# Kernel tuning notes

Measured on AMD Instinct MI355X. Metric: run time of the kernel, lower is better.

The kernel has to match this reference:

```python
import jax, jax.numpy as jnp
import numpy as np

B, C_I, C_O, K, H, W = 8, 64, 64, 3, 256, 256
GROUPS = 16  # int(c_o / min(4, c_o)) = 64/4
EPS = 1e-5
PAD = K  # pad_x = pad_y = k + (bc-1) with bc_x=bc_y=1, k=3


def _conv(x, w):
    # x: (B, C_i, h, w), w: (C_o, C_i, K, K), valid conv, stride 1
    return jax.lax.conv_general_dilated(
        x, w, window_strides=(1, 1), padding='VALID',
        dimension_numbers=('NCHW', 'OIHW', 'NCHW'))


def setup_inputs() -> dict:
    key = jax.random.key(0)
    ks = jax.random.split(key, 10)
    s = 1.0 / np.sqrt(C_I * K * K)  # torch Conv2d default init bound
    wshape = (C_O, C_I, K, K)
    names = ['w_int', 'w_tl', 'w_tr', 'w_bl', 'w_br', 'w_top', 'w_bot', 'w_left', 'w_right']
    d = {'x': jax.random.normal(ks[0], (B, C_I, H, W), dtype=jnp.float32)}
    for i, n in enumerate(names):
        d[n] = jax.random.uniform(ks[i + 1], wshape, jnp.float32, -s, s)
    d['bias'] = jnp.zeros((1, C_O, 1, 1), jnp.float32)   # learnable_bias (init zeros)
    d['gamma'] = jnp.ones((C_O,), jnp.float32)           # GroupNorm weight
    d['beta'] = jnp.zeros((C_O,), jnp.float32)           # GroupNorm bias
    return d


def reference(x, w_int, w_tl, w_tr, w_bl, w_br, w_top, w_bot, w_left, w_right, bias, gamma, beta):
    p = PAD
    # corners -> (B,C,1,1)
    tl = _conv(x[:, :, :p, :p], w_tl)
    tr = _conv(x[:, :, :p, -p:], w_tr)
    bl = _conv(x[:, :, -p:, :p], w_bl)
    br = _conv(x[:, :, -p:, -p:], w_br)
    # edges -> (B,C,1,W-2) / (B,C,H-2,1)
    top = _conv(x[:, :, :p, :], w_top)
    bot = _conv(x[:, :, -p:, :], w_bot)
    left = _conv(x[:, :, :, :p], w_left)
    right = _conv(x[:, :, :, -p:], w_right)
    # interior -> (B,C,H-2,W-2)
    mid = _conv(x, w_int)
    mid = jnp.concatenate([left, mid, right], axis=3)       # (B,C,H-2,W)
    top_row = jnp.concatenate([tl, top, tr], axis=3)        # (B,C,1,W)
    bot_row = jnp.concatenate([bl, bot, br], axis=3)        # (B,C,1,W)
    # NOTE: original code puts the 'bottom' conv output first along dim 2
    y = jnp.concatenate([bot_row, mid, top_row], axis=2) + bias  # (B,C,H,W)
    # GroupNorm(16, 64)
    yg = y.reshape(B, GROUPS, -1)
    mu = jnp.mean(yg, axis=2, keepdims=True)
    var = jnp.var(yg, axis=2, keepdims=True)
    yn = ((yg - mu) * jax.lax.rsqrt(var + EPS)).reshape(B, C_O, H, W)
    yn = yn * gamma[None, :, None, None] + beta[None, :, None, None]
    # SELU activation; dropout(rate=0) is identity
    return jax.nn.selu(yn)
```

## Files before the change

### kernel.cpp

```cpp
#include <hip/hip_runtime.h>

#define B_ 8
#define CI 64
#define CO 64
#define H_ 256
#define W_ 256
#define EPS_ 1e-5f

#define SELU_SCALE 1.0507009873554805f
#define SELU_SA    1.7580993408473766f

typedef __attribute__((ext_vector_type(8))) short short8;
typedef __attribute__((ext_vector_type(4))) float f32x4;
typedef unsigned int u32;

__device__ __forceinline__ unsigned short f2bf(float f) {
    unsigned int u = __float_as_uint(f);
    u = (u + 0x7fffu + ((u >> 16) & 1u)) >> 16;
    return (unsigned short)u;
}
__device__ __forceinline__ float bf2f(unsigned short h) {
    return __uint_as_float(((unsigned)h) << 16);
}
__device__ __forceinline__ float selu_f(float u) {
    return (u > 0.f) ? SELU_SCALE * u : SELU_SA * (__expf(u) - 1.f);
}
__device__ __forceinline__ void gload_lds16(const void* g, void* l) {
    __builtin_amdgcn_global_load_lds(
        (const __attribute__((address_space(1))) u32*)g,
        (__attribute__((address_space(3))) u32*)l, 16, 0, 0);
}

__global__ __launch_bounds__(256) void prepass_weights(
    const float* __restrict__ w_int,
    const float* __restrict__ w_bl, const float* __restrict__ w_br,
    const float* __restrict__ w_tl, const float* __restrict__ w_tr,
    const float* __restrict__ w_bot, const float* __restrict__ w_top,
    const float* __restrict__ w_left, const float* __restrict__ w_right,
    unsigned short* __restrict__ wpre, float* __restrict__ wedge)
{
    const int blk = blockIdx.x, t = threadIdx.x;
    if (blk < 72) {
        const int wid = blk / 9, pos = blk % 9;
        const float* src = (wid == 0) ? w_bl : (wid == 1) ? w_br
                         : (wid == 2) ? w_tl : (wid == 3) ? w_tr
                         : (wid == 4) ? w_bot : (wid == 5) ? w_top
                         : (wid == 6) ? w_left : w_right;
        float* dst = wedge + (size_t)blk * 4096;
        for (int k = 0; k < 16; ++k) {
            const int lin = k * 256 + t;
            const int c4  = lin >> 8;
            const int co  = (lin >> 2) & 63;
            const int j   = lin & 3;
            const int ci  = c4 * 4 + j;
            dst[lin] = src[(co * 64 + ci) * 9 + pos];
        }
    } else {
        const int pos = blk - 72;
        for (int k = 0; k < 16; ++k) {
            const int lin = k * 256 + t;
            const int co = lin >> 6, cip = lin & 63;
            const int ci = cip ^ ((co & 7) << 3);
            wpre[pos * 4096 + lin] = f2bf(w_int[(co * 64 + ci) * 9 + pos]);
        }
    }
}

__global__ __launch_bounds__(256) void prepass_x(
    const float* __restrict__ x, unsigned short* __restrict__ xpre)
{
    __shared__ unsigned short ls[256 * 72];
    const int row = blockIdx.x, b = blockIdx.y;
    const int t = threadIdx.x;
    const int colq = t >> 2;
    const float* xb = x + ((size_t)(b * 64) * 256 + row) * 256;

    for (int sp = 0; sp < 4; ++sp) {
        const int cibase = sp * 16 + (t & 3) * 4;
        float4 v[4];
#pragma unroll
        for (int e = 0; e < 4; ++e)
            v[e] = *(const float4*)(xb + (size_t)(cibase + e) * 65536 + colq * 4);
#pragma unroll
        for (int jj = 0; jj < 4; ++jj) {
            const int col = colq * 4 + jj;
            const int sw  = (col & 7) << 3;
            ushort4 pk;
            pk.x = f2bf((&v[0].x)[jj]);
            pk.y = f2bf((&v[1].x)[jj]);
            pk.z = f2bf((&v[2].x)[jj]);
            pk.w = f2bf((&v[3].x)[jj]);
            *(ushort4*)&ls[col * 72 + (cibase ^ sw)] = pk;
        }
    }
    __syncthreads();
    unsigned short* xp = xpre + ((size_t)(b * 256 + row)) * 256 * 64;
    for (int q = 0; q < 8; ++q) {
        const int lin = q * 256 + t;
        const int col = lin >> 3, k = lin & 7;
        *(uint4*)(xp + col * 64 + k * 8) = *(const uint4*)&ls[col * 72 + k * 8];
    }
}

__global__ __launch_bounds__(512, 4) void conv_mfma(
    const unsigned short* __restrict__ xpre, const unsigned short* __restrict__ wpre,
    const float* __restrict__ bias, unsigned short* __restrict__ ybf,
    float* __restrict__ part)
{
    __shared__ unsigned short xs[10 * 48 * 64];
    __shared__ float sred[8][16][2];
    const int t = threadIdx.x, w = t >> 6, lane = t & 63;
    const int b = blockIdx.z, r0 = blockIdx.y * 8, c0 = blockIdx.x * 32;

    for (int L = w; L < 60; L += 8) {
        const int j = L / 6, i = L % 6;
        int rr = r0 - 1 + j; rr = rr < 0 ? 0 : (rr > 255 ? 255 : rr);
        int col = c0 - 8 + i * 8 + (lane >> 3);
        col = col < 0 ? 0 : (col > 255 ? 255 : col);
        const char* src = (const char*)xpre +
            ((size_t)((b * 256 + rr) * 256 + col)) * 128 + (lane & 7) * 16;
        gload_lds16(src, (char*)xs + j * 6144 + i * 1024);
    }

    const int l15 = lane & 15, lg = lane >> 4;
    const int sw15 = (l15 & 7) << 3;

    int jb[3];
#pragma unroll
    for (int kr = 0; kr < 3; ++kr) jb[kr] = (w + kr) * 6144;
    int offb[3][2][2];
#pragma unroll
    for (int kc = 0; kc < 3; ++kc)
#pragma unroll
        for (int n = 0; n < 2; ++n) {
            const int s = n * 16 + l15 + kc + 7;
#pragma unroll
            for (int ks = 0; ks < 2; ++ks) {
                const int cib = ks * 32 + lg * 8;
                offb[kc][n][ks] = s * 128 + ((cib ^ ((s & 7) << 3)) << 1);
            }
        }
    const char* pw[2];
#pragma unroll
    for (int ks = 0; ks < 2; ++ks) {
        const int cib = ks * 32 + lg * 8;
        pw[ks] = (const char*)wpre + l15 * 128 + ((cib ^ sw15) << 1);
    }

    f32x4 acc[4][2];
#pragma unroll
    for (int m = 0; m < 4; ++m)
#pragma unroll
        for (int n = 0; n < 2; ++n)
            acc[m][n] = (f32x4){0.f, 0.f, 0.f, 0.f};

    __syncthreads();

    short8 afr[2][4];
#pragma unroll
    for (int m = 0; m < 4; ++m)
        afr[0][m] = *(const short8*)(pw[0] + m * 2048);

#pragma unroll
    for (int lin = 0; lin < 18; ++lin) {
        const int pos = lin >> 1, ks = lin & 1;
        const int kr = pos / 3, kc = pos % 3;
        if (lin < 17) {
            const int lin1 = lin + 1;
            const int pos1 = lin1 >> 1, ks1 = lin1 & 1;
#pragma unroll
            for (int m = 0; m < 4; ++m)
                afr[lin1 & 1][m] =
                    *(const short8*)(pw[ks1] + pos1 * 8192 + m * 2048);
        }
        short8 bf[2];
#pragma unroll
        for (int n = 0; n < 2; ++n)
            bf[n] = *(const short8*)((const char*)xs + jb[kr] + offb[kc][n][ks]);
#pragma unroll
        for (int m = 0; m < 4; ++m)
#pragma unroll
            for (int n = 0; n < 2; ++n)
                acc[m][n] = __builtin_amdgcn_mfma_f32_16x16x32_bf16(
                    afr[lin & 1][m], bf[n], acc[m][n], 0, 0, 0);
    }

    const int r = r0 + w;
    const bool rmask = (r != 0) && (r != 255);
    float s4[4] = {0.f, 0.f, 0.f, 0.f}, q4[4] = {0.f, 0.f, 0.f, 0.f};
#pragma unroll
    for (int m = 0; m < 4; ++m)
#pragma unroll
        for (int n = 0; n < 2; ++n) {
            const int c = c0 + n * 16 + l15;
            const bool pmask = rmask && (c != 0) && (c != 255);
#pragma unroll
            for (int reg = 0; reg < 4; ++reg) {
                const int co = m * 16 + lg * 4 + reg;
                const float v = acc[m][n][reg] + bias[co];
                ybf[(((size_t)b * 64 + co) * 256 + r) * 256 + c] = f2bf(v);
                if (pmask) { s4[m] += v; q4[m] += v * v; }
            }
        }
#pragma unroll
    for (int off = 1; off < 16; off <<= 1)
#pragma unroll
        for (int m = 0; m < 4; ++m) {
            s4[m] += __shfl_xor(s4[m], off);
            q4[m] += __shfl_xor(q4[m], off);
        }
    if (l15 == 0) {
#pragma unroll
        for (int m = 0; m < 4; ++m) {
            sred[w][m * 4 + lg][0] = s4[m];
            sred[w][m * 4 + lg][1] = q4[m];
        }
    }
    __syncthreads();
    if (t < 32) {
        const int g = t & 15, sel = t >> 4;
        float v = 0.f;
#pragma unroll
        for (int ww = 0; ww < 8; ++ww) v += sred[ww][g][sel];
        const int slot = blockIdx.y * 8 + blockIdx.x;
        part[((size_t)(b * 512 + slot) * 16 + g) * 2 + sel] = v;
    }
}

__global__ __launch_bounds__(256) void conv_edge2(
    const unsigned short* __restrict__ xpre, const float* __restrict__ wedge,
    const float* __restrict__ bias, unsigned short* __restrict__ ybf,
    float* __restrict__ part)
{
    __shared__ float xl[4][9][64];
    __shared__ float ered[4][16][2];
    const int b = blockIdx.x, edge = blockIdx.y, seg = blockIdx.z;
    const int t = threadIdx.x, p = t >> 6, lane = t & 63;

    for (int unit = t; unit < 288; unit += 256) {
        const int chunk = unit >> 3, sub = unit & 7;
        const int pp = chunk / 9, rem = chunk % 9, kr = rem / 3, kc = rem % 3;
        int e = seg * 4 + pp;
        if (edge >= 2 && e > 253) e = 253;
        int row, colb;
        if (edge == 0)      { row = 253 + kr; colb = (e == 0) ? 0 : ((e == 255) ? 253 : (e - 1)); }
        else if (edge == 1) { row = kr;       colb = (e == 0) ? 0 : ((e == 255) ? 253 : (e - 1)); }
        else if (edge == 2) { row = e + kr;   colb = 0; }
        else                { row = e + kr;   colb = 253; }
        const int col = colb + kc;
        const uint4 v = *(const uint4*)(xpre +
            ((size_t)((b * 256 + row) * 256 + col)) * 64 + sub * 8);
        const int ci0 = (sub ^ (col & 7)) * 8;
        float* dst = &xl[pp][kr * 3 + kc][ci0];
        const unsigned short* hv = (const unsigned short*)&v;
#pragma unroll
        for (int j = 0; j < 8; ++j) dst[j] = bf2f(hv[j]);
    }
    __syncthreads();

    int e = seg * 4 + p;
    const bool active = (edge < 2) || (e <= 253);
    if (edge >= 2 && e > 253) e = 253;
    int wid, r_out, c_out;
    if (edge == 0)      { wid = (e == 0) ? 0 : ((e == 255) ? 1 : 4); r_out = 0;   c_out = e; }
    else if (edge == 1) { wid = (e == 0) ? 2 : ((e == 255) ? 3 : 5); r_out = 255; c_out = e; }
    else if (edge == 2) { wid = 6; r_out = e + 1; c_out = 0; }
    else                { wid = 7; r_out = e + 1; c_out = 255; }

    const int co = lane;
    float acc = 0.f;
    const float* wbase = wedge + (size_t)wid * 36864;
#pragma unroll
    for (int pos = 0; pos < 9; ++pos) {
        const float* wp = wbase + pos * 4096 + lane * 4;
        const float* xp = &xl[p][pos][0];
#pragma unroll
        for (int c4 = 0; c4 < 16; ++c4) {
            const float4 wv = *(const float4*)(wp + c4 * 256);
            const float4 xv = *(const float4*)(xp + c4 * 4);
            acc = fmaf(wv.x, xv.x, acc); acc = fmaf(wv.y, xv.y, acc);
            acc = fmaf(wv.z, xv.z, acc); acc = fmaf(wv.w, xv.w, acc);
        }
    }
    const float v = acc + bias[co];
    if (active) ybf[(((size_t)b * 64 + co) * 256 + r_out) * 256 + c_out] = f2bf(v);
    float s = active ? v : 0.f, q = active ? v * v : 0.f;
    s += __shfl_xor(s, 1); q += __shfl_xor(q, 1);
    s += __shfl_xor(s, 2); q += __shfl_xor(q, 2);
    if ((lane & 3) == 0) { ered[p][co >> 2][0] = s; ered[p][co >> 2][1] = q; }
    __syncthreads();
    if (t < 32) {
        const int g = t & 15, sel = t >> 4;
        const float r = ered[0][g][sel] + ered[1][g][sel] +
                        ered[2][g][sel] + ered[3][g][sel];
        const int slot = 256 + (edge * 64 + seg);
        part[((size_t)(b * 512 + slot) * 16 + g) * 2 + sel] = r;
    }
}

__global__ __launch_bounds__(256) void stats_reduce(
    const float* __restrict__ part, float* __restrict__ mv)
{
    __shared__ float sred[16][16][2];
    const int b = blockIdx.x, t = threadIdx.x;
    const int g = t & 15, chunk = t >> 4;
    float s = 0.f, q = 0.f;
    for (int k = 0; k < 32; ++k) {
        const int slot = chunk * 32 + k;
        const size_t base = ((size_t)(b * 512 + slot) * 16 + g) * 2;
        s += part[base]; q += part[base + 1];
    }
    sred[chunk][g][0] = s; sred[chunk][g][1] = q;
    __syncthreads();
    if (t < 16) {
        float S = 0.f, Q = 0.f;
#pragma unroll
        for (int c = 0; c < 16; ++c) { S += sred[c][t][0]; Q += sred[c][t][1]; }
        const float inv_n = 1.0f / (4.0f * 65536.0f);
        const float mean = S * inv_n;
        const float var  = Q * inv_n - mean * mean;
        mv[(b * 16 + t) * 2]     = mean;
        mv[(b * 16 + t) * 2 + 1] = rsqrtf(var + EPS_);
    }
}

__global__ __launch_bounds__(256) void norm_bf(
    const unsigned short* __restrict__ ybf, float* __restrict__ out,
    const float* __restrict__ mv,
    const float* __restrict__ gamma, const float* __restrict__ beta)
{
    const size_t tt = (size_t)blockIdx.x * 256 + threadIdx.x;
    const size_t e = tt * 8;
    const int b  = (int)(e >> 22);
    const int ch = (int)((e >> 16) & 63);
    const int g  = ch >> 2;
    const float mean = mv[(b * 16 + g) * 2];
    const float rstd = mv[(b * 16 + g) * 2 + 1];
    const float ga = gamma[ch] * rstd;
    const float be = beta[ch] - mean * ga;

    const uint4 v = *(const uint4*)(ybf + e);
    float f[8];
    f[0] = __uint_as_float(v.x << 16); f[1] = __uint_as_float(v.x & 0xffff0000u);
    f[2] = __uint_as_float(v.y << 16); f[3] = __uint_as_float(v.y & 0xffff0000u);
    f[4] = __uint_as_float(v.z << 16); f[5] = __uint_as_float(v.z & 0xffff0000u);
    f[6] = __uint_as_float(v.w << 16); f[7] = __uint_as_float(v.w & 0xffff0000u);
    float4 o0, o1;
    o0.x = selu_f(f[0] * ga + be); o0.y = selu_f(f[1] * ga + be);
    o0.z = selu_f(f[2] * ga + be); o0.w = selu_f(f[3] * ga + be);
    o1.x = selu_f(f[4] * ga + be); o1.y = selu_f(f[5] * ga + be);
    o1.z = selu_f(f[6] * ga + be); o1.w = selu_f(f[7] * ga + be);
    *(float4*)(out + e)     = o0;
    *(float4*)(out + e + 4) = o1;
}

__global__ __launch_bounds__(256) void conv_main(
    const float* __restrict__ x, const float* __restrict__ w,
    const float* __restrict__ bias, float* __restrict__ y)
{
    const int c = threadIdx.x;
    const int r = blockIdx.x;
    const int b = blockIdx.y;
    const int rr = (r == 0) ? (H_ - 3) : ((r == H_ - 1) ? 0 : (r - 1));
    const int cc = min(max(c - 1, 0), W_ - 3);
    float acc[CO];
#pragma unroll
    for (int co = 0; co < CO; ++co) acc[co] = 0.f;
    const float* xb = x + (size_t)b * CI * H_ * W_;
    for (int ci = 0; ci < CI; ++ci) {
        const float* xp = xb + ((size_t)ci * H_ + rr) * W_ + cc;
        float xv[9];
#pragma unroll
        for (int kr = 0; kr < 3; ++kr)
#pragma unroll
            for (int kc = 0; kc < 3; ++kc)
                xv[kr * 3 + kc] = xp[kr * W_ + kc];
        const float* wci = w + ci * 9;
#pragma unroll
        for (int co = 0; co < CO; ++co) {
            const float* wp = wci + co * (CI * 9);
            float a = acc[co];
#pragma unroll
            for (int k = 0; k < 9; ++k) a = fmaf(xv[k], wp[k], a);
            acc[co] = a;
        }
    }
#pragma unroll
    for (int co = 0; co < CO; ++co)
        y[(((size_t)b * CO + co) * H_ + r) * W_ + c] = acc[co] + bias[co];
}

__global__ __launch_bounds__(256) void conv_edge(
    const float* __restrict__ x,
    const float* __restrict__ w_bot, const float* __restrict__ w_top,
    const float* __restrict__ w_left, const float* __restrict__ w_right,
    const float* __restrict__ bias, float* __restrict__ y)
{
    const int b     = blockIdx.x;
    const int edge  = blockIdx.y;
    const int seg   = blockIdx.z;
    const int el    = threadIdx.x & 63;
    const int chunk = threadIdx.x >> 6;
    const int e     = seg * 64 + el;
    const bool active = (e < 254);
    const int ec    = active ? e : 253;
    const float* w = (edge == 0) ? w_bot : (edge == 1) ? w_top
                   : (edge == 2) ? w_left : w_right;
    int r_out, c_out, rr, cc;
    if (edge == 0)      { r_out = 0;      c_out = 1 + ec; rr = H_ - 3; cc = ec; }
    else if (edge == 1) { r_out = H_ - 1; c_out = 1 + ec; rr = 0;      cc = ec; }
    else if (edge == 2) { r_out = 1 + ec; c_out = 0;      rr = ec;     cc = 0; }
    else                { r_out = 1 + ec; c_out = W_ - 1; rr = ec;     cc = W_ - 3; }
    float acc[CO];
#pragma unroll
    for (int co = 0; co < CO; ++co) acc[co] = 0.f;
    const float* xb = x + (size_t)b * CI * H_ * W_;
    const int ci0 = chunk * 16;
    for (int ci = ci0; ci < ci0 + 16; ++ci) {
        const float* xp = xb + ((size_t)ci * H_ + rr) * W_ + cc;
        float xv[9];
#pragma unroll
        for (int kr = 0; kr < 3; ++kr)
#pragma unroll
            for (int kc = 0; kc < 3; ++kc)
                xv[kr * 3 + kc] = xp[kr * W_ + kc];
#pragma unroll
        for (int co = 0; co < CO; ++co) {
            const float* wp = w + co * (CI * 9) + ci * 9;
            float a = acc[co];
#pragma unroll
            for (int k = 0; k < 9; ++k) a = fmaf(xv[k], wp[k], a);
            acc[co] = a;
        }
    }
    __shared__ float lds[64][65];
    for (int s = 0; s < 4; ++s) {
        if (chunk == s) {
            if (s == 0) {
#pragma unroll
                for (int co = 0; co < CO; ++co) lds[el][co] = acc[co];
            } else {
#pragma unroll
                for (int co = 0; co < CO; ++co) lds[el][co] += acc[co];
            }
        }
        __syncthreads();
    }
    if (chunk == 0 && active) {
#pragma unroll
        for (int co = 0; co < CO; ++co)
            y[(((size_t)b * CO + co) * H_ + r_out) * W_ + c_out] = lds[el][co] + bias[co];
    }
}

__global__ __launch_bounds__(256) void conv_corner(
    const float* __restrict__ x,
    const float* __restrict__ w_bl, const float* __restrict__ w_br,
    const float* __restrict__ w_tl, const float* __restrict__ w_tr,
    const float* __restrict__ bias, float* __restrict__ y)
{
    const int b      = blockIdx.x;
    const int corner = threadIdx.x >> 6;
    const int co     = threadIdx.x & 63;
    const float* w = (corner == 0) ? w_bl : (corner == 1) ? w_br
                   : (corner == 2) ? w_tl : w_tr;
    const int rr    = (corner < 2) ? (H_ - 3) : 0;
    const int cc    = (corner & 1) ? (W_ - 3) : 0;
    const int r_out = (corner < 2) ? 0 : (H_ - 1);
    const int c_out = (corner & 1) ? (W_ - 1) : 0;
    const float* xb = x + (size_t)b * CI * H_ * W_;
    float a = 0.f;
    for (int ci = 0; ci < CI; ++ci) {
        const float* xp = xb + ((size_t)ci * H_ + rr) * W_ + cc;
        const float* wp = w + ((size_t)co * CI + ci) * 9;
#pragma unroll
        for (int kr = 0; kr < 3; ++kr)
#pragma unroll
            for (int kc = 0; kc < 3; ++kc)
                a = fmaf(xp[kr * W_ + kc], wp[kr * 3 + kc], a);
    }
    y[(((size_t)b * CO + co) * H_ + r_out) * W_ + c_out] = a + bias[co];
}

__global__ __launch_bounds__(256) void stats_kernel(
    const float* __restrict__ y, float* __restrict__ ws)
{
    const int bid   = blockIdx.x;
    const int chunk = bid & 3;
    const int g     = (bid >> 2) & 15;
    const int b     = bid >> 6;
    const float* p  = y + ((size_t)(b * 64 + g * 4 + chunk)) * (H_ * W_);
    float s = 0.f, q = 0.f;
    for (int i = threadIdx.x; i < (H_ * W_ / 4); i += 256) {
        float4 v = reinterpret_cast<const float4*>(p)[i];
        s += v.x + v.y + v.z + v.w;
        q += v.x * v.x + v.y * v.y + v.z * v.z + v.w * v.w;
    }
#pragma unroll
    for (int off = 32; off; off >>= 1) {
        s += __shfl_down(s, off);
        q += __shfl_down(q, off);
    }
    __shared__ float red[8];
    const int wid = threadIdx.x >> 6;
    if ((threadIdx.x & 63) == 0) { red[wid * 2] = s; red[wid * 2 + 1] = q; }
    __syncthreads();
    if (threadIdx.x == 0) {
        ws[bid * 2]     = red[0] + red[2] + red[4] + red[6];
        ws[bid * 2 + 1] = red[1] + red[3] + red[5] + red[7];
    }
}

__global__ __launch_bounds__(256) void norm_stats(
    float* __restrict__ y, const float* __restrict__ st,
    const float* __restrict__ gamma, const float* __restrict__ beta)
{
    const size_t t = (size_t)blockIdx.x * 256 + threadIdx.x;
    const size_t e = t * 4;
    const int b  = (int)(e >> 22);
    const int ch = (int)((e >> 16) & 63);
    const int g  = ch >> 2;
    const int sb = ((b * 16 + g) * 4) * 2;
    const float S = st[sb] + st[sb + 2] + st[sb + 4] + st[sb + 6];
    const float Q = st[sb + 1] + st[sb + 3] + st[sb + 5] + st[sb + 7];
    const float inv_n = 1.0f / (4.0f * H_ * W_);
    const float mean  = S * inv_n;
    const float var   = Q * inv_n - mean * mean;
    const float rstd  = rsqrtf(var + EPS_);
    const float ga = gamma[ch] * rstd;
    const float be = beta[ch] - mean * ga;
    float4 v = reinterpret_cast<float4*>(y)[t];
    float u;
    u = v.x * ga + be; v.x = selu_f(u);
    u = v.y * ga + be; v.y = selu_f(u);
    u = v.z * ga + be; v.z = selu_f(u);
    u = v.w * ga + be; v.w = selu_f(u);
    reinterpret_cast<float4*>(y)[t] = v;
}

extern "C" void kernel_launch(void* const* d_in, const int* in_sizes, int n_in,
                              void* d_out, int out_size, void* d_ws, size_t ws_size,
                              hipStream_t stream) {
    const float* x       = (const float*)d_in[0];
    const float* w_int   = (const float*)d_in[1];
    const float* w_tl    = (const float*)d_in[2];
    const float* w_tr    = (const float*)d_in[3];
    const float* w_bl    = (const float*)d_in[4];
    const float* w_br    = (const float*)d_in[5];
    const float* w_top   = (const float*)d_in[6];
    const float* w_bot   = (const float*)d_in[7];
    const float* w_left  = (const float*)d_in[8];
    const float* w_right = (const float*)d_in[9];
    const float* bias    = (const float*)d_in[10];
    const float* gamma   = (const float*)d_in[11];
    const float* beta    = (const float*)d_in[12];

    float* out = (float*)d_out;

    const size_t XPRE  = 67108864ull;
    const size_t YBF   = 67108864ull;
    const size_t WPRE  = 73728ull;
    const size_t WEDGE = 1179648ull;
    const size_t PART  = 524288ull;
    const size_t MV    = 1024ull;
    const size_t NEED  = XPRE + YBF + WPRE + WEDGE + PART + MV;

    if (ws_size >= NEED) {
        unsigned short* xpre = (unsigned short*)d_ws;
        unsigned short* ybf  = (unsigned short*)((char*)d_ws + XPRE);
        unsigned short* wpre = (unsigned short*)((char*)d_ws + XPRE + YBF);
        float* wedge = (float*)((char*)d_ws + XPRE + YBF + WPRE);
        float* part  = (float*)((char*)d_ws + XPRE + YBF + WPRE + WEDGE);
        float* mv    = (float*)((char*)d_ws + XPRE + YBF + WPRE + WEDGE + PART);

        prepass_weights<<<dim3(81), 256, 0, stream>>>(
            w_int, w_bl, w_br, w_tl, w_tr, w_bot, w_top, w_left, w_right, wpre, wedge);
        prepass_x<<<dim3(256, 8), 256, 0, stream>>>(x, xpre);
        conv_mfma<<<dim3(8, 32, 8), 512, 0, stream>>>(xpre, wpre, bias, ybf, part);
        conv_edge2<<<dim3(8, 4, 64), 256, 0, stream>>>(xpre, wedge, bias, ybf, part);
        stats_reduce<<<dim3(8), 256, 0, stream>>>(part, mv);
        norm_bf<<<dim3(16384), 256, 0, stream>>>(ybf, out, mv, gamma, beta);
    } else {
        float* stats = (float*)d_ws;
        conv_main<<<dim3(H_, B_), 256, 0, stream>>>(x, w_int, bias, out);
        conv_edge<<<dim3(B_, 4, 4), 256, 0, stream>>>(x, w_bot, w_top, w_left, w_right, bias, out);
        conv_corner<<<dim3(B_), 256, 0, stream>>>(x, w_bl, w_br, w_tl, w_tr, bias, out);
        stats_kernel<<<dim3(512), 256, 0, stream>>>(out, stats);
        norm_stats<<<dim3(32768), 256, 0, stream>>>(out, stats, gamma, beta);
    }
}
```

Baseline: 200.7 us.

## Stage conv weights through double-buffered LDS instead of per-wave global loads

Weights for each kernel tap are now fetched cooperatively into a two-slot LDS buffer with async global-to-LDS loads, prefetching the next tap while the current one is consumed. Before, every wave loaded its weight fragments directly from global memory. The aim is to cut redundant global and L2 traffic across the 8 waves. In exchange it adds a block-wide barrier per tap and extra LDS reads, which may lower occupancy given the launch bounds.

```diff
diff --git a/kernel.cpp b/kernel.cpp
--- a/kernel.cpp
+++ b/kernel.cpp
@@ -108,6 +108,7 @@
     float* __restrict__ part)
 {
     __shared__ unsigned short xs[10 * 48 * 64];
+    __shared__ unsigned short wl2[2][4096];
     __shared__ float sred[8][16][2];
     const int t = threadIdx.x, w = t >> 6, lane = t & 63;
     const int b = blockIdx.z, r0 = blockIdx.y * 8, c0 = blockIdx.x * 32;
@@ -121,6 +122,8 @@
             ((size_t)((b * 256 + rr) * 256 + col)) * 128 + (lane & 7) * 16;
         gload_lds16(src, (char*)xs + j * 6144 + i * 1024);
     }
+    gload_lds16((const char*)wpre + w * 1024 + lane * 16,
+                (char*)wl2[0] + w * 1024);
 
     const int l15 = lane & 15, lg = lane >> 4;
     const int sw15 = (l15 & 7) << 3;
@@ -140,12 +143,14 @@
                 offb[kc][n][ks] = s * 128 + ((cib ^ ((s & 7) << 3)) << 1);
             }
         }
-    const char* pw[2];
-#pragma unroll
-    for (int ks = 0; ks < 2; ++ks) {
-        const int cib = ks * 32 + lg * 8;
-        pw[ks] = (const char*)wpre + l15 * 128 + ((cib ^ sw15) << 1);
-    }
+    int afo[2][4];
+#pragma unroll
+    for (int ks = 0; ks < 2; ++ks)
+#pragma unroll
+        for (int m = 0; m < 4; ++m) {
+            const int cib = ks * 32 + lg * 8;
+            afo[ks][m] = (m * 16 + l15) * 128 + ((cib ^ sw15) << 1);
+        }
 
     f32x4 acc[4][2];
 #pragma unroll
@@ -156,33 +161,31 @@
 
     __syncthreads();
 
-    short8 afr[2][4];
-#pragma unroll
-    for (int m = 0; m < 4; ++m)
-        afr[0][m] = *(const short8*)(pw[0] + m * 2048);
-
-#pragma unroll
-    for (int lin = 0; lin < 18; ++lin) {
-        const int pos = lin >> 1, ks = lin & 1;
+#pragma unroll
+    for (int pos = 0; pos < 9; ++pos) {
+        const int cur = pos & 1;
+        if (pos < 8)
+            gload_lds16((const char*)wpre + (pos + 1) * 8192 + w * 1024 + lane * 16,
+                        (char*)wl2[cur ^ 1] + w * 1024);
         const int kr = pos / 3, kc = pos % 3;
-        if (lin < 17) {
-            const int lin1 = lin + 1;
-            const int pos1 = lin1 >> 1, ks1 = lin1 & 1;
+        const char* wbuf = (const char*)wl2[cur];
+#pragma unroll
+        for (int ks = 0; ks < 2; ++ks) {
+            short8 bf[2], af[4];
+#pragma unroll
+            for (int n = 0; n < 2; ++n)
+                bf[n] = *(const short8*)((const char*)xs + jb[kr] + offb[kc][n][ks]);
 #pragma unroll
             for (int m = 0; m < 4; ++m)
-                afr[lin1 & 1][m] =
-                    *(const short8*)(pw[ks1] + pos1 * 8192 + m * 2048);
-        }
-        short8 bf[2];
-#pragma unroll
-        for (int n = 0; n < 2; ++n)
-            bf[n] = *(const short8*)((const char*)xs + jb[kr] + offb[kc][n][ks]);
-#pragma unroll
-        for (int m = 0; m < 4; ++m)
-#pragma unroll
-            for (int n = 0; n < 2; ++n)
-                acc[m][n] = __builtin_amdgcn_mfma_f32_16x16x32_bf16(
-                    afr[lin & 1][m], bf[n], acc[m][n], 0, 0, 0);
+                af[m] = *(const short8*)(wbuf + afo[ks][m]);
+#pragma unroll
+            for (int m = 0; m < 4; ++m)
+#pragma unroll
+                for (int n = 0; n < 2; ++n)
+                    acc[m][n] = __builtin_amdgcn_mfma_f32_16x16x32_bf16(
+                        af[m], bf[n], acc[m][n], 0, 0, 0);
+        }
+        __syncthreads();
     }
 
     const int r = r0 + w;
```

After: 180.6 us. 1.11x faster.
